# Performance work log

Hardware: AMD Instinct MI355X
Metric: run time of the kernel (lower is better)

Reference implementation:

```python
import jax, jax.numpy as jnp
import numpy as np

B, S, D_IN, D_OUT, H = 4, 2048, 1024, 1024, 16
HD = D_OUT // H  # head_dim = 64


def setup_inputs() -> dict:
    key = jax.random.key(0)
    ks = jax.random.split(key, 6)
    scale = 1.0 / np.sqrt(D_IN)
    return {
        "x": jax.random.normal(ks[0], (B, S, D_IN), dtype=jnp.float32),
        "Wq": jax.random.normal(ks[1], (D_IN, D_OUT), dtype=jnp.float32) * scale,
        "Wk": jax.random.normal(ks[2], (D_IN, D_OUT), dtype=jnp.float32) * scale,
        "Wv": jax.random.normal(ks[3], (D_IN, D_OUT), dtype=jnp.float32) * scale,
        "Wo": jax.random.normal(ks[4], (D_OUT, D_OUT), dtype=jnp.float32) * (1.0 / np.sqrt(D_OUT)),
        "bo": jax.random.normal(ks[5], (D_OUT,), dtype=jnp.float32) * 0.02,
    }


def reference(x, Wq, Wk, Wv, Wo, bo):
    b, n, _ = x.shape
    h, hd = H, HD
    # projections -> (b, h, n, hd)
    q = (x @ Wq).reshape(b, n, h, hd).transpose(0, 2, 1, 3)
    k = (x @ Wk).reshape(b, n, h, hd).transpose(0, 2, 1, 3)
    v = (x @ Wv).reshape(b, n, h, hd).transpose(0, 2, 1, 3)
    # scores (b, h, n, n) with causal mask then scale (matches original order)
    scores = jnp.einsum("bhqd,bhkd->bhqk", q, k)
    causal = jnp.tril(jnp.ones((n, n), dtype=bool))  # True = keep
    scores = jnp.where(causal, scores, -jnp.inf) / jnp.sqrt(jnp.asarray(hd, x.dtype))
    attn = jax.nn.softmax(scores, axis=-1)
    ctx = jnp.einsum("bhqk,bhkd->bhqd", attn, v)
    ctx = ctx.transpose(0, 2, 1, 3).reshape(b, n, h * hd)
    return ctx @ Wo + bo
```

## Files before the change

### kernel.cpp

```cpp
#include <hip/hip_runtime.h>
#include <hip/hip_bf16.h>
#include <math.h>

typedef __attribute__((ext_vector_type(4))) float f32x4;
typedef __attribute__((ext_vector_type(16))) float f32x16;
typedef __attribute__((ext_vector_type(8))) short bf16x8;
typedef __attribute__((ext_vector_type(4))) unsigned int u32x4;

#define DEV __device__ __forceinline__
#define MFMA16 __builtin_amdgcn_mfma_f32_16x16x32_bf16
#define MFMA32 __builtin_amdgcn_mfma_f32_32x32x16_bf16
#define SBAR __builtin_amdgcn_s_barrier()
#define SCHED0 __builtin_amdgcn_sched_barrier(0)

constexpr int S      = 2048;
constexpr int DMODEL = 1024;
constexpr int HD     = 64;
constexpr int MROWS  = 4 * 2048;

DEV unsigned short f2bf(float f) {
  union { float f; unsigned int u; } v; v.f = f;
  unsigned int u = v.u;
  unsigned int r = u + 0x7fffu + ((u >> 16) & 1u);
  return (unsigned short)(r >> 16);
}

DEV unsigned int pkbf(float lo, float hi) {
  __hip_bfloat162 h = __float22bfloat162_rn(float2{lo, hi});
  union { __hip_bfloat162 h; unsigned int u; } c; c.h = h;
  return c.u;
}

DEV void gload_lds16(const void* g, void* l) {
  __builtin_amdgcn_global_load_lds(
      (const __attribute__((address_space(1))) unsigned int*)g,
      (__attribute__((address_space(3))) unsigned int*)l, 16, 0, 0);
}

__global__ __launch_bounds__(256) void k_conv(const float* __restrict__ in,
                                              unsigned short* __restrict__ out) {
  int i = blockIdx.x * 256 + threadIdx.x;
  float4 v = ((const float4*)in)[i];
  ushort4 o;
  o.x = f2bf(v.x); o.y = f2bf(v.y); o.z = f2bf(v.z); o.w = f2bf(v.w);
  ((ushort4*)out)[i] = o;
}

__global__ __launch_bounds__(256) void k_transpose(const float* __restrict__ W,
                                                   unsigned short* __restrict__ Wt) {
  __shared__ float tile[32][33];
  int n0 = blockIdx.x * 32, k0 = blockIdx.y * 32;
  int tx = threadIdx.x, ty = threadIdx.y;
#pragma unroll
  for (int j = 0; j < 4; ++j)
    tile[ty + j * 8][tx] = W[(size_t)(k0 + ty + j * 8) * DMODEL + n0 + tx];
  __syncthreads();
#pragma unroll
  for (int j = 0; j < 4; ++j)
    Wt[(size_t)(n0 + ty + j * 8) * DMODEL + k0 + tx] = f2bf(tile[tx][ty + j * 8]);
}

template<int NBX, int EPI>
__global__ __launch_bounds__(512, 2) void k_gemm8(const unsigned short* __restrict__ A,
                                                  const unsigned short* __restrict__ Bt,
                                                  unsigned short* __restrict__ Qg,
                                                  unsigned short* __restrict__ Kg,
                                                  unsigned short* __restrict__ Vg,
                                                  const float* __restrict__ bo,
                                                  float* __restrict__ out) {
  __shared__ __align__(16) char lds[98304];
  const int tid = threadIdx.x, lane = tid & 63;
  const int wid = tid >> 6, wm = wid >> 1, wn = wid & 1;
  const int lq = lane & 15, lg = lane >> 4;
  const int flat = blockIdx.x;
  const int wg = (flat & 7) * (NBX * 4) + (flat >> 3);
  const int by = wg / NBX, bx = wg % NBX;
  const int m0 = by * 256, n0 = bx * 128;

  auto stage = [&](int kt, int buf) {
    char* dA = lds + buf * 49152;
    char* dB = dA + 32768;
    const unsigned short* gA = A + (size_t)m0 * DMODEL + kt * 64;
    const unsigned short* gB = Bt + (size_t)n0 * DMODEL + kt * 64;
#pragma unroll
    for (int i = 0; i < 4; ++i) {
      int c = tid + i * 512; int r = c >> 3, cc = c & 7;
      gload_lds16(gA + (size_t)r * DMODEL + ((cc ^ (r & 7)) << 3), dA + c * 16);
    }
#pragma unroll
    for (int i = 0; i < 2; ++i) {
      int c = tid + i * 512; int r = c >> 3, cc = c & 7;
      gload_lds16(gB + (size_t)r * DMODEL + ((cc ^ (r & 7)) << 3), dB + c * 16);
    }
  };

  stage(0, 0);
  stage(1, 1);
  SCHED0;
  asm volatile("s_waitcnt vmcnt(6)" ::: "memory");
  SCHED0;
  SBAR;
  SCHED0;

  f32x4 acc[4][4] = {};
#pragma unroll 1
  for (int t = 0; t < 16; ++t) {
    const int cur = t & 1;
    const char* pA = lds + cur * 49152;
    const char* pB = pA + 32768;
    bf16x8 af[4][2], bf[4][2];
#pragma unroll
    for (int kk = 0; kk < 2; ++kk) {
#pragma unroll
      for (int mi = 0; mi < 4; ++mi) {
        int row = wm * 64 + mi * 16 + lq;
        af[mi][kk] = *(const bf16x8*)(pA + row * 128 + ((((kk << 2) + lg) ^ (row & 7)) << 4));
      }
#pragma unroll
      for (int ni = 0; ni < 4; ++ni) {
        int row = wn * 64 + ni * 16 + lq;
        bf[ni][kk] = *(const bf16x8*)(pB + row * 128 + ((((kk << 2) + lg) ^ (row & 7)) << 4));
      }
    }
    asm volatile("s_waitcnt lgkmcnt(0)" ::: "memory");
    SCHED0;
    SBAR;
    SCHED0;
    if (t < 14) stage(t + 2, cur);
    __builtin_amdgcn_s_setprio(1);
#pragma unroll
    for (int kk = 0; kk < 2; ++kk)
#pragma unroll
      for (int mi = 0; mi < 4; ++mi)
#pragma unroll
        for (int ni = 0; ni < 4; ++ni)
          acc[mi][ni] = MFMA16(af[mi][kk], bf[ni][kk], acc[mi][ni], 0, 0, 0);
    __builtin_amdgcn_s_setprio(0);
    SCHED0;
    if (t < 14) {
      asm volatile("s_waitcnt vmcnt(6)" ::: "memory");
    } else if (t == 14) {
      asm volatile("s_waitcnt vmcnt(0)" ::: "memory");
    }
    SCHED0;
    SBAR;
    SCHED0;
  }

  if (EPI == 0) {
#pragma unroll
    for (int mi = 0; mi < 4; ++mi)
#pragma unroll
      for (int ni = 0; ni < 4; ++ni) {
        int n = n0 + wn * 64 + ni * 16 + lq;
        int widx = n >> 10, nn = n & 1023;
        int h = nn >> 6, d = nn & 63;
        unsigned short* dst = (widx == 0) ? Qg : ((widx == 1) ? Kg : Vg);
        float scale = (widx == 0) ? 0.125f : 1.0f;
#pragma unroll
        for (int r = 0; r < 4; ++r) {
          int m = m0 + wm * 64 + mi * 16 + lg * 4 + r;
          int b_ = m >> 11, s_ = m & 2047;
          dst[(size_t)((b_ * 16 + h) * 2048 + s_) * HD + d] = f2bf(acc[mi][ni][r] * scale);
        }
      }
  } else {
#pragma unroll
    for (int mi = 0; mi < 4; ++mi)
#pragma unroll
      for (int ni = 0; ni < 4; ++ni) {
        int n = n0 + wn * 64 + ni * 16 + lq;
        float bv = bo[n];
#pragma unroll
        for (int r = 0; r < 4; ++r) {
          int m = m0 + wm * 64 + mi * 16 + lg * 4 + r;
          out[(size_t)m * DMODEL + n] = acc[mi][ni][r] + bv;
        }
      }
  }
}

__global__ __launch_bounds__(512, 2) void k_attn(const unsigned short* __restrict__ Qg,
                                                 const unsigned short* __restrict__ Kg,
                                                 const unsigned short* __restrict__ Vg,
                                                 unsigned short* __restrict__ Ctx) {
  __shared__ __align__(16) char lds[32768];
  const int pr = blockIdx.x;
  const int bh = blockIdx.y;
  const int tid = threadIdx.x;
  const int lane = tid & 63, w = tid >> 6;
  const int lq5 = lane & 31, hi = lane >> 5;
  const size_t base = (size_t)bh * (S * HD);
  const int b = bh >> 4, h = bh & 15;
  const int vkrow = tid >> 3, vcc = tid & 7;

#pragma unroll 1
  for (int half = 0; half < 2; ++half) {
    const int Qb = half ? (7 - pr) : pr;
    const int q0w = Qb * 256 + w * 32;
    const int tmax = 4 * Qb + 3;
    const int diag = q0w >> 6;

    bf16x8 qF[4];
#pragma unroll
    for (int dc = 0; dc < 4; ++dc)
      qF[dc] = *(const bf16x8*)(Qg + base + (size_t)(q0w + lq5) * HD + dc * 16 + hi * 8);

    f32x16 o0 = {}, o1 = {};
    float m_run = -INFINITY, l_run = 0.f;

    __syncthreads();
    {
      int row = tid >> 3, cc = tid & 7, scc = cc ^ (row & 7);
      gload_lds16(Kg + base + (size_t)row * HD + scc * 8, lds + tid * 16);
      bf16x8 vv = *(const bf16x8*)(Vg + base + (size_t)vkrow * HD + vcc * 8);
#pragma unroll
      for (int j = 0; j < 8; ++j) {
        int d = vcc * 8 + j;
        int fd = (d & 7) ^ ((d >> 3) & 7);
        *(unsigned short*)(lds + 16384 + d * 128 + (((vkrow >> 3) ^ fd) << 4) + (vkrow & 7) * 2) =
            (unsigned short)vv[j];
      }
    }
    __syncthreads();

#pragma unroll 1
    for (int t = 0; t <= tmax; ++t) {
      const int cur = t & 1, nxt = cur ^ 1;
      char* sK  = lds + cur * 8192;
      char* sVT = lds + 16384 + cur * 8192;
      const bool have_next = (t < tmax);
      bf16x8 vv;
      if (have_next) {
        vv = *(const bf16x8*)(Vg + base + (size_t)((t + 1) * 64 + vkrow) * HD + vcc * 8);
        int row = tid >> 3, cc = tid & 7, scc = cc ^ (row & 7);
        gload_lds16(Kg + base + (size_t)((t + 1) * 64 + row) * HD + scc * 8,
                    lds + nxt * 8192 + tid * 16);
      }
      const bool active = (t <= diag);
      if (active) {
        const bool isdiag = (t == diag);
        const int nkb = (isdiag && !(q0w & 32)) ? 1 : 2;
        f32x16 st0 = {}, st1 = {};
#pragma unroll
        for (int dc = 0; dc < 4; ++dc) {
          int row = lq5;
          bf16x8 a0 = *(const bf16x8*)(sK + row * 128 + (((2 * dc + hi) ^ (row & 7)) << 4));
          st0 = MFMA32(a0, qF[dc], st0, 0, 0, 0);
        }
        if (nkb == 2) {
#pragma unroll
          for (int dc = 0; dc < 4; ++dc) {
            int row = 32 + lq5;
            bf16x8 a1 = *(const bf16x8*)(sK + row * 128 + (((2 * dc + hi) ^ (row & 7)) << 4));
            st1 = MFMA32(a1, qF[dc], st1, 0, 0, 0);
          }
        }
        if (isdiag) {
          int qo = q0w + lq5 - t * 64;
          if (q0w & 32) {
#pragma unroll
            for (int r = 0; r < 16; ++r) {
              int key = 32 + (r & 3) + 8 * (r >> 2) + 4 * hi;
              st1[r] = (key > qo) ? -INFINITY : st1[r];
            }
          } else {
#pragma unroll
            for (int r = 0; r < 16; ++r) {
              int key = (r & 3) + 8 * (r >> 2) + 4 * hi;
              st0[r] = (key > qo) ? -INFINITY : st0[r];
            }
          }
        }
        float mx = st0[0];
#pragma unroll
        for (int r = 1; r < 16; ++r) mx = fmaxf(mx, st0[r]);
        if (nkb == 2) {
#pragma unroll
          for (int r = 0; r < 16; ++r) mx = fmaxf(mx, st1[r]);
        }
        mx = fmaxf(mx, __shfl_xor(mx, 32));
        bool need = !(mx <= m_run + 8.0f);
        if (__any(need)) {
          float mn = fmaxf(m_run, mx);
          float alpha = __expf(m_run - mn);
          m_run = mn;
          l_run *= alpha;
#pragma unroll
          for (int r = 0; r < 16; ++r) { o0[r] *= alpha; o1[r] *= alpha; }
        }
        float rs[4] = {0.f, 0.f, 0.f, 0.f};
#pragma unroll
        for (int r = 0; r < 16; ++r) {
          float p = __expf(st0[r] - m_run);
          st0[r] = p;
          rs[r & 3] += p;
        }
        if (nkb == 2) {
#pragma unroll
          for (int r = 0; r < 16; ++r) {
            float p = __expf(st1[r] - m_run);
            st1[r] = p;
            rs[r & 3] += p;
          }
        }
        float rsum = (rs[0] + rs[1]) + (rs[2] + rs[3]);
        rsum += __shfl_xor(rsum, 32);
        l_run += rsum;
        {
          unsigned int wv[8];
#pragma unroll
          for (int j = 0; j < 8; ++j) wv[j] = pkbf(st0[2 * j], st0[2 * j + 1]);
          asm("v_permlane32_swap_b32 %0, %1" : "+v"(wv[0]), "+v"(wv[2]));
          asm("v_permlane32_swap_b32 %0, %1" : "+v"(wv[1]), "+v"(wv[3]));
          asm("v_permlane32_swap_b32 %0, %1" : "+v"(wv[4]), "+v"(wv[6]));
          asm("v_permlane32_swap_b32 %0, %1" : "+v"(wv[5]), "+v"(wv[7]));
          union { bf16x8 v; unsigned int u[4]; } fa, fb;
          fa.u[0] = wv[0]; fa.u[1] = wv[1]; fa.u[2] = wv[2]; fa.u[3] = wv[3];
          fb.u[0] = wv[4]; fb.u[1] = wv[5]; fb.u[2] = wv[6]; fb.u[3] = wv[7];
#pragma unroll
          for (int kc = 0; kc < 2; ++kc) {
            bf16x8 bp = kc ? fb.v : fa.v;
            {
              int d = lq5, fd = (d & 7) ^ ((d >> 3) & 7);
              bf16x8 av = *(const bf16x8*)(sVT + d * 128 + (((kc * 2 + hi) ^ fd) << 4));
              o0 = MFMA32(av, bp, o0, 0, 0, 0);
            }
            {
              int d = 32 + lq5, fd = (d & 7) ^ ((d >> 3) & 7);
              bf16x8 av = *(const bf16x8*)(sVT + d * 128 + (((kc * 2 + hi) ^ fd) << 4));
              o1 = MFMA32(av, bp, o1, 0, 0, 0);
            }
          }
        }
        if (nkb == 2) {
          unsigned int wv[8];
#pragma unroll
          for (int j = 0; j < 8; ++j) wv[j] = pkbf(st1[2 * j], st1[2 * j + 1]);
          asm("v_permlane32_swap_b32 %0, %1" : "+v"(wv[0]), "+v"(wv[2]));
          asm("v_permlane32_swap_b32 %0, %1" : "+v"(wv[1]), "+v"(wv[3]));
          asm("v_permlane32_swap_b32 %0, %1" : "+v"(wv[4]), "+v"(wv[6]));
          asm("v_permlane32_swap_b32 %0, %1" : "+v"(wv[5]), "+v"(wv[7]));
          union { bf16x8 v; unsigned int u[4]; } fa, fb;
          fa.u[0] = wv[0]; fa.u[1] = wv[1]; fa.u[2] = wv[2]; fa.u[3] = wv[3];
          fb.u[0] = wv[4]; fb.u[1] = wv[5]; fb.u[2] = wv[6]; fb.u[3] = wv[7];
#pragma unroll
          for (int kc = 0; kc < 2; ++kc) {
            bf16x8 bp = kc ? fb.v : fa.v;
            {
              int d = lq5, fd = (d & 7) ^ ((d >> 3) & 7);
              bf16x8 av = *(const bf16x8*)(sVT + d * 128 + ((((2 + kc) * 2 + hi) ^ fd) << 4));
              o0 = MFMA32(av, bp, o0, 0, 0, 0);
            }
            {
              int d = 32 + lq5, fd = (d & 7) ^ ((d >> 3) & 7);
              bf16x8 av = *(const bf16x8*)(sVT + d * 128 + ((((2 + kc) * 2 + hi) ^ fd) << 4));
              o1 = MFMA32(av, bp, o1, 0, 0, 0);
            }
          }
        }
      }
      if (have_next) {
        char* dVT = lds + 16384 + nxt * 8192;
#pragma unroll
        for (int j = 0; j < 8; ++j) {
          int d = vcc * 8 + j;
          int fd = (d & 7) ^ ((d >> 3) & 7);
          *(unsigned short*)(dVT + d * 128 + (((vkrow >> 3) ^ fd) << 4) + (vkrow & 7) * 2) =
              (unsigned short)vv[j];
        }
      }
      __syncthreads();
    }

    __syncthreads();
    {
      float inv = 1.0f / l_run;
      char* slice = lds + w * 4096;
#pragma unroll
      for (int db = 0; db < 2; ++db)
#pragma unroll
        for (int j = 0; j < 8; ++j) {
          int d0 = (j & 1) * 2 + (j >> 1) * 8 + 4 * hi + 32 * db;
          float va = (db ? o1[2 * j] : o0[2 * j]) * inv;
          float vb = (db ? o1[2 * j + 1] : o0[2 * j + 1]) * inv;
          *(unsigned int*)(slice + lq5 * 128 + (((d0 >> 3) ^ (lq5 & 7)) << 4) + (d0 & 7) * 2) =
              pkbf(va, vb);
        }
      asm volatile("s_waitcnt lgkmcnt(0)" ::: "memory");
#pragma unroll
      for (int i = 0; i < 4; ++i) {
        int r = lane >> 1, cc = (lane & 1) * 4 + i;
        u32x4 v = *(const u32x4*)(slice + r * 128 + ((cc ^ (r & 7)) << 4));
        *(u32x4*)(Ctx + (size_t)(b * S + q0w + r) * DMODEL + h * HD + cc * 8) = v;
      }
    }
  }
}

extern "C" void kernel_launch(void* const* d_in, const int* in_sizes, int n_in,
                              void* d_out, int out_size, void* d_ws, size_t ws_size,
                              hipStream_t stream) {
  const float* x  = (const float*)d_in[0];
  const float* Wq = (const float*)d_in[1];
  const float* Wk = (const float*)d_in[2];
  const float* Wv = (const float*)d_in[3];
  const float* Wo = (const float*)d_in[4];
  const float* bo = (const float*)d_in[5];
  float* out = (float*)d_out;

  char* p = (char*)d_ws;
  unsigned short* xb  = (unsigned short*)p; p += (size_t)MROWS * DMODEL * 2;
  unsigned short* wt  = (unsigned short*)p; p += (size_t)3 * DMODEL * DMODEL * 2;
  unsigned short* wot = (unsigned short*)p; p += (size_t)DMODEL * DMODEL * 2;
  unsigned short* qg  = (unsigned short*)p; p += (size_t)MROWS * DMODEL * 2;
  unsigned short* kg  = (unsigned short*)p; p += (size_t)MROWS * DMODEL * 2;
  unsigned short* vg  = (unsigned short*)p; p += (size_t)MROWS * DMODEL * 2;
  unsigned short* ctx = (unsigned short*)p; p += (size_t)MROWS * DMODEL * 2;

  k_conv<<<(MROWS * DMODEL) / 1024, 256, 0, stream>>>(x, xb);
  dim3 tb(32, 8), tg(32, 32);
  k_transpose<<<tg, tb, 0, stream>>>(Wq, wt);
  k_transpose<<<tg, tb, 0, stream>>>(Wk, wt + (size_t)DMODEL * DMODEL);
  k_transpose<<<tg, tb, 0, stream>>>(Wv, wt + (size_t)2 * DMODEL * DMODEL);
  k_transpose<<<tg, tb, 0, stream>>>(Wo, wot);
  k_gemm8<24, 0><<<768, 512, 0, stream>>>(xb, wt, qg, kg, vg, nullptr, nullptr);
  k_attn<<<dim3(4, 64), 512, 0, stream>>>(qg, kg, vg, ctx);
  k_gemm8<8, 1><<<256, 512, 0, stream>>>(ctx, wot, nullptr, nullptr, nullptr, bo, out);
}
```

Baseline: 192.1 us.

## Split attention blocks into half-size CTAs, use exp2 softmax, raise MFMA priority

The attention kernel moves from 512-thread blocks over 256 query rows to 256-thread blocks over 128 query rows, launching twice as many blocks. Each thread now loads two K/V chunks per tile. The aim is finer load balance across the causal triangle and higher occupancy, at the cost of each block reloading K/V tiles that used to be shared by twice as many queries. The Q scale now folds in log2(e) so softmax can use exp2f, and s_setprio brackets the MFMA sections to favour matrix issue across waves.

```diff
diff --git a/kernel.cpp b/kernel.cpp
--- a/kernel.cpp
+++ b/kernel.cpp
@@ -156,7 +156,7 @@
         int widx = n >> 10, nn = n & 1023;
         int h = nn >> 6, d = nn & 63;
         unsigned short* dst = (widx == 0) ? Qg : ((widx == 1) ? Kg : Vg);
-        float scale = (widx == 0) ? 0.125f : 1.0f;
+        float scale = (widx == 0) ? 0.18033688f : 1.0f;
 #pragma unroll
         for (int r = 0; r < 4; ++r) {
           int m = m0 + wm * 64 + mi * 16 + lg * 4 + r;
@@ -180,24 +180,24 @@
   }
 }
 
-__global__ __launch_bounds__(512, 2) void k_attn(const unsigned short* __restrict__ Qg,
+__global__ __launch_bounds__(256, 4) void k_attn(const unsigned short* __restrict__ Qg,
                                                  const unsigned short* __restrict__ Kg,
                                                  const unsigned short* __restrict__ Vg,
                                                  unsigned short* __restrict__ Ctx) {
   __shared__ __align__(16) char lds[32768];
-  const int pr = blockIdx.x;
+  const int pr = blockIdx.x >> 1;
+  const int sub = blockIdx.x & 1;
   const int bh = blockIdx.y;
   const int tid = threadIdx.x;
   const int lane = tid & 63, w = tid >> 6;
   const int lq5 = lane & 31, hi = lane >> 5;
   const size_t base = (size_t)bh * (S * HD);
   const int b = bh >> 4, h = bh & 15;
-  const int vkrow = tid >> 3, vcc = tid & 7;
 
 #pragma unroll 1
   for (int half = 0; half < 2; ++half) {
     const int Qb = half ? (7 - pr) : pr;
-    const int q0w = Qb * 256 + w * 32;
+    const int q0w = Qb * 256 + sub * 128 + w * 32;
     const int tmax = 4 * Qb + 3;
     const int diag = q0w >> 6;
 
@@ -210,15 +210,22 @@
     float m_run = -INFINITY, l_run = 0.f;
 
     __syncthreads();
-    {
-      int row = tid >> 3, cc = tid & 7, scc = cc ^ (row & 7);
-      gload_lds16(Kg + base + (size_t)row * HD + scc * 8, lds + tid * 16);
-      bf16x8 vv = *(const bf16x8*)(Vg + base + (size_t)vkrow * HD + vcc * 8);
+#pragma unroll
+    for (int i = 0; i < 2; ++i) {
+      int c = tid + i * 256;
+      int row = c >> 3, cc = c & 7, scc = cc ^ (row & 7);
+      gload_lds16(Kg + base + (size_t)row * HD + scc * 8, lds + c * 16);
+    }
+#pragma unroll
+    for (int i = 0; i < 2; ++i) {
+      int c = tid + i * 256;
+      int krow = c >> 3, vcc = c & 7;
+      bf16x8 vv = *(const bf16x8*)(Vg + base + (size_t)krow * HD + vcc * 8);
 #pragma unroll
       for (int j = 0; j < 8; ++j) {
         int d = vcc * 8 + j;
         int fd = (d & 7) ^ ((d >> 3) & 7);
-        *(unsigned short*)(lds + 16384 + d * 128 + (((vkrow >> 3) ^ fd) << 4) + (vkrow & 7) * 2) =
+        *(unsigned short*)(lds + 16384 + d * 128 + (((krow >> 3) ^ fd) << 4) + (krow & 7) * 2) =
             (unsigned short)vv[j];
       }
     }
@@ -230,18 +237,28 @@
       char* sK  = lds + cur * 8192;
       char* sVT = lds + 16384 + cur * 8192;
       const bool have_next = (t < tmax);
-      bf16x8 vv;
+      bf16x8 vv[2];
       if (have_next) {
-        vv = *(const bf16x8*)(Vg + base + (size_t)((t + 1) * 64 + vkrow) * HD + vcc * 8);
-        int row = tid >> 3, cc = tid & 7, scc = cc ^ (row & 7);
-        gload_lds16(Kg + base + (size_t)((t + 1) * 64 + row) * HD + scc * 8,
-                    lds + nxt * 8192 + tid * 16);
+#pragma unroll
+        for (int i = 0; i < 2; ++i) {
+          int c = tid + i * 256;
+          int krow = c >> 3, vcc = c & 7;
+          vv[i] = *(const bf16x8*)(Vg + base + (size_t)((t + 1) * 64 + krow) * HD + vcc * 8);
+        }
+#pragma unroll
+        for (int i = 0; i < 2; ++i) {
+          int c = tid + i * 256;
+          int row = c >> 3, cc = c & 7, scc = cc ^ (row & 7);
+          gload_lds16(Kg + base + (size_t)((t + 1) * 64 + row) * HD + scc * 8,
+                      lds + nxt * 8192 + c * 16);
+        }
       }
       const bool active = (t <= diag);
       if (active) {
         const bool isdiag = (t == diag);
         const int nkb = (isdiag && !(q0w & 32)) ? 1 : 2;
         f32x16 st0 = {}, st1 = {};
+        __builtin_amdgcn_s_setprio(1);
 #pragma unroll
         for (int dc = 0; dc < 4; ++dc) {
           int row = lq5;
@@ -256,6 +273,7 @@
             st1 = MFMA32(a1, qF[dc], st1, 0, 0, 0);
           }
         }
+        __builtin_amdgcn_s_setprio(0);
         if (isdiag) {
           int qo = q0w + lq5 - t * 64;
           if (q0w & 32) {
@@ -283,7 +301,7 @@
         bool need = !(mx <= m_run + 8.0f);
         if (__any(need)) {
           float mn = fmaxf(m_run, mx);
-          float alpha = __expf(m_run - mn);
+          float alpha = exp2f(m_run - mn);
           m_run = mn;
           l_run *= alpha;
 #pragma unroll
@@ -292,14 +310,14 @@
         float rs[4] = {0.f, 0.f, 0.f, 0.f};
 #pragma unroll
         for (int r = 0; r < 16; ++r) {
-          float p = __expf(st0[r] - m_run);
+          float p = exp2f(st0[r] - m_run);
           st0[r] = p;
           rs[r & 3] += p;
         }
         if (nkb == 2) {
 #pragma unroll
           for (int r = 0; r < 16; ++r) {
-            float p = __expf(st1[r] - m_run);
+            float p = exp2f(st1[r] - m_run);
             st1[r] = p;
             rs[r & 3] += p;
           }
@@ -318,6 +336,7 @@
           union { bf16x8 v; unsigned int u[4]; } fa, fb;
           fa.u[0] = wv[0]; fa.u[1] = wv[1]; fa.u[2] = wv[2]; fa.u[3] = wv[3];
           fb.u[0] = wv[4]; fb.u[1] = wv[5]; fb.u[2] = wv[6]; fb.u[3] = wv[7];
+          __builtin_amdgcn_s_setprio(1);
 #pragma unroll
           for (int kc = 0; kc < 2; ++kc) {
             bf16x8 bp = kc ? fb.v : fa.v;
@@ -332,6 +351,7 @@
               o1 = MFMA32(av, bp, o1, 0, 0, 0);
             }
           }
+          __builtin_amdgcn_s_setprio(0);
         }
         if (nkb == 2) {
           unsigned int wv[8];
@@ -344,6 +364,7 @@
           union { bf16x8 v; unsigned int u[4]; } fa, fb;
           fa.u[0] = wv[0]; fa.u[1] = wv[1]; fa.u[2] = wv[2]; fa.u[3] = wv[3];
           fb.u[0] = wv[4]; fb.u[1] = wv[5]; fb.u[2] = wv[6]; fb.u[3] = wv[7];
+          __builtin_amdgcn_s_setprio(1);
 #pragma unroll
           for (int kc = 0; kc < 2; ++kc) {
             bf16x8 bp = kc ? fb.v : fa.v;
@@ -358,16 +379,22 @@
               o1 = MFMA32(av, bp, o1, 0, 0, 0);
             }
           }
+          __builtin_amdgcn_s_setprio(0);
         }
       }
       if (have_next) {
         char* dVT = lds + 16384 + nxt * 8192;
 #pragma unroll
-        for (int j = 0; j < 8; ++j) {
-          int d = vcc * 8 + j;
-          int fd = (d & 7) ^ ((d >> 3) & 7);
-          *(unsigned short*)(dVT + d * 128 + (((vkrow >> 3) ^ fd) << 4) + (vkrow & 7) * 2) =
-              (unsigned short)vv[j];
+        for (int i = 0; i < 2; ++i) {
+          int c = tid + i * 256;
+          int krow = c >> 3, vcc = c & 7;
+#pragma unroll
+          for (int j = 0; j < 8; ++j) {
+            int d = vcc * 8 + j;
+            int fd = (d & 7) ^ ((d >> 3) & 7);
+            *(unsigned short*)(dVT + d * 128 + (((krow >> 3) ^ fd) << 4) + (krow & 7) * 2) =
+                (unsigned short)vv[i][j];
+          }
         }
       }
       __syncthreads();
@@ -425,6 +452,6 @@
   k_transpose<<<tg, tb, 0, stream>>>(Wv, wt + (size_t)2 * DMODEL * DMODEL);
   k_transpose<<<tg, tb, 0, stream>>>(Wo, wot);
   k_gemm8<24, 0><<<768, 512, 0, stream>>>(xb, wt, qg, kg, vg, nullptr, nullptr);
-  k_attn<<<dim3(4, 64), 512, 0, stream>>>(qg, kg, vg, ctx);
+  k_attn<<<dim3(8, 64), 256, 0, stream>>>(qg, kg, vg, ctx);
   k_gemm8<8, 1><<<256, 512, 0, stream>>>(ctx, wot, nullptr, nullptr, nullptr, bo, out);
 }
```

Measured after the change: 317.1 us. 1.65x slower.

## Use 1024-thread attention blocks with split K/V loaders, exp2 softmax and MFMA priority

Applied to the files above, without the earlier changes.

Attention blocks now hold 16 waves covering a 512-row query block, replacing the previous scheme where each block processed two paired 256-row halves in sequence. The K tile is loaded by the first half of the threads and the V tile is transposed into LDS by the second half. The Q scale now folds in log2(e), so the softmax uses exp2f instead of __expf, and s_setprio brackets raise wave priority around the MFMA sections. This removes the causal load-balancing pairing, so blocks with larger query indices carry more work, and blocks are now twice as large.

```diff
diff --git a/kernel.cpp b/kernel.cpp
--- a/kernel.cpp
+++ b/kernel.cpp
@@ -156,7 +156,7 @@
         int widx = n >> 10, nn = n & 1023;
         int h = nn >> 6, d = nn & 63;
         unsigned short* dst = (widx == 0) ? Qg : ((widx == 1) ? Kg : Vg);
-        float scale = (widx == 0) ? 0.125f : 1.0f;
+        float scale = (widx == 0) ? 0.18033688f : 1.0f;
 #pragma unroll
         for (int r = 0; r < 4; ++r) {
           int m = m0 + wm * 64 + mi * 16 + lg * 4 + r;
@@ -180,220 +180,226 @@
   }
 }
 
-__global__ __launch_bounds__(512, 2) void k_attn(const unsigned short* __restrict__ Qg,
-                                                 const unsigned short* __restrict__ Kg,
-                                                 const unsigned short* __restrict__ Vg,
-                                                 unsigned short* __restrict__ Ctx) {
-  __shared__ __align__(16) char lds[32768];
-  const int pr = blockIdx.x;
+__global__ __launch_bounds__(1024, 4) void k_attn(const unsigned short* __restrict__ Qg,
+                                                  const unsigned short* __restrict__ Kg,
+                                                  const unsigned short* __restrict__ Vg,
+                                                  unsigned short* __restrict__ Ctx) {
+  __shared__ __align__(16) char lds[65536];
+  const int Qb = blockIdx.x;
   const int bh = blockIdx.y;
   const int tid = threadIdx.x;
   const int lane = tid & 63, w = tid >> 6;
   const int lq5 = lane & 31, hi = lane >> 5;
   const size_t base = (size_t)bh * (S * HD);
   const int b = bh >> 4, h = bh & 15;
-  const int vkrow = tid >> 3, vcc = tid & 7;
+
+  const bool isV = (tid >= 512);
+  const int c = tid & 511;
+  const int krow = c >> 3, cc = c & 7;
+  const int scc = cc ^ (krow & 7);
+
+  const int q0w = Qb * 512 + w * 32;
+  const int tmax = 8 * Qb + 7;
+  const int diag = q0w >> 6;
+
+  bf16x8 qF[4];
+#pragma unroll
+  for (int dc = 0; dc < 4; ++dc)
+    qF[dc] = *(const bf16x8*)(Qg + base + (size_t)(q0w + lq5) * HD + dc * 16 + hi * 8);
+
+  f32x16 o0 = {}, o1 = {};
+  float m_run = -INFINITY, l_run = 0.f;
+
+  if (!isV) {
+    gload_lds16(Kg + base + (size_t)krow * HD + scc * 8, lds + c * 16);
+  } else {
+    bf16x8 vv = *(const bf16x8*)(Vg + base + (size_t)krow * HD + cc * 8);
+#pragma unroll
+    for (int j = 0; j < 8; ++j) {
+      int d = cc * 8 + j;
+      int fd = (d & 7) ^ ((d >> 3) & 7);
+      *(unsigned short*)(lds + 16384 + d * 128 + (((krow >> 3) ^ fd) << 4) + (krow & 7) * 2) =
+          (unsigned short)vv[j];
+    }
+  }
+  __syncthreads();
 
 #pragma unroll 1
-  for (int half = 0; half < 2; ++half) {
-    const int Qb = half ? (7 - pr) : pr;
-    const int q0w = Qb * 256 + w * 32;
-    const int tmax = 4 * Qb + 3;
-    const int diag = q0w >> 6;
-
-    bf16x8 qF[4];
-#pragma unroll
-    for (int dc = 0; dc < 4; ++dc)
-      qF[dc] = *(const bf16x8*)(Qg + base + (size_t)(q0w + lq5) * HD + dc * 16 + hi * 8);
-
-    f32x16 o0 = {}, o1 = {};
-    float m_run = -INFINITY, l_run = 0.f;
-
+  for (int t = 0; t <= tmax; ++t) {
+    const int cur = t & 1, nxt = cur ^ 1;
+    char* sK  = lds + cur * 8192;
+    char* sVT = lds + 16384 + cur * 8192;
+    const bool have_next = (t < tmax);
+    bf16x8 vv;
+    if (have_next) {
+      if (!isV)
+        gload_lds16(Kg + base + (size_t)((t + 1) * 64 + krow) * HD + scc * 8,
+                    lds + nxt * 8192 + c * 16);
+      else
+        vv = *(const bf16x8*)(Vg + base + (size_t)((t + 1) * 64 + krow) * HD + cc * 8);
+    }
+    const bool active = (t <= diag);
+    if (active) {
+      const bool isdiag = (t == diag);
+      const int nkb = (isdiag && !(q0w & 32)) ? 1 : 2;
+      f32x16 st0 = {}, st1 = {};
+      __builtin_amdgcn_s_setprio(1);
+#pragma unroll
+      for (int dc = 0; dc < 4; ++dc) {
+        int row = lq5;
+        bf16x8 a0 = *(const bf16x8*)(sK + row * 128 + (((2 * dc + hi) ^ (row & 7)) << 4));
+        st0 = MFMA32(a0, qF[dc], st0, 0, 0, 0);
+      }
+      if (nkb == 2) {
+#pragma unroll
+        for (int dc = 0; dc < 4; ++dc) {
+          int row = 32 + lq5;
+          bf16x8 a1 = *(const bf16x8*)(sK + row * 128 + (((2 * dc + hi) ^ (row & 7)) << 4));
+          st1 = MFMA32(a1, qF[dc], st1, 0, 0, 0);
+        }
+      }
+      __builtin_amdgcn_s_setprio(0);
+      if (isdiag) {
+        int qo = q0w + lq5 - t * 64;
+        if (q0w & 32) {
+#pragma unroll
+          for (int r = 0; r < 16; ++r) {
+            int key = 32 + (r & 3) + 8 * (r >> 2) + 4 * hi;
+            st1[r] = (key > qo) ? -INFINITY : st1[r];
+          }
+        } else {
+#pragma unroll
+          for (int r = 0; r < 16; ++r) {
+            int key = (r & 3) + 8 * (r >> 2) + 4 * hi;
+            st0[r] = (key > qo) ? -INFINITY : st0[r];
+          }
+        }
+      }
+      float mx = st0[0];
+#pragma unroll
+      for (int r = 1; r < 16; ++r) mx = fmaxf(mx, st0[r]);
+      if (nkb == 2) {
+#pragma unroll
+        for (int r = 0; r < 16; ++r) mx = fmaxf(mx, st1[r]);
+      }
+      mx = fmaxf(mx, __shfl_xor(mx, 32));
+      bool need = !(mx <= m_run + 8.0f);
+      if (__any(need)) {
+        float mn = fmaxf(m_run, mx);
+        float alpha = exp2f(m_run - mn);
+        m_run = mn;
+        l_run *= alpha;
+#pragma unroll
+        for (int r = 0; r < 16; ++r) { o0[r] *= alpha; o1[r] *= alpha; }
+      }
+      float rs[4] = {0.f, 0.f, 0.f, 0.f};
+#pragma unroll
+      for (int r = 0; r < 16; ++r) {
+        float p = exp2f(st0[r] - m_run);
+        st0[r] = p;
+        rs[r & 3] += p;
+      }
+      if (nkb == 2) {
+#pragma unroll
+        for (int r = 0; r < 16; ++r) {
+          float p = exp2f(st1[r] - m_run);
+          st1[r] = p;
+          rs[r & 3] += p;
+        }
+      }
+      float rsum = (rs[0] + rs[1]) + (rs[2] + rs[3]);
+      rsum += __shfl_xor(rsum, 32);
+      l_run += rsum;
+      {
+        unsigned int wv[8];
+#pragma unroll
+        for (int j = 0; j < 8; ++j) wv[j] = pkbf(st0[2 * j], st0[2 * j + 1]);
+        asm("v_permlane32_swap_b32 %0, %1" : "+v"(wv[0]), "+v"(wv[2]));
+        asm("v_permlane32_swap_b32 %0, %1" : "+v"(wv[1]), "+v"(wv[3]));
+        asm("v_permlane32_swap_b32 %0, %1" : "+v"(wv[4]), "+v"(wv[6]));
+        asm("v_permlane32_swap_b32 %0, %1" : "+v"(wv[5]), "+v"(wv[7]));
+        union { bf16x8 v; unsigned int u[4]; } fa, fb;
+        fa.u[0] = wv[0]; fa.u[1] = wv[1]; fa.u[2] = wv[2]; fa.u[3] = wv[3];
+        fb.u[0] = wv[4]; fb.u[1] = wv[5]; fb.u[2] = wv[6]; fb.u[3] = wv[7];
+        __builtin_amdgcn_s_setprio(1);
+#pragma unroll
+        for (int kc = 0; kc < 2; ++kc) {
+          bf16x8 bp = kc ? fb.v : fa.v;
+          {
+            int d = lq5, fd = (d & 7) ^ ((d >> 3) & 7);
+            bf16x8 av = *(const bf16x8*)(sVT + d * 128 + (((kc * 2 + hi) ^ fd) << 4));
+            o0 = MFMA32(av, bp, o0, 0, 0, 0);
+          }
+          {
+            int d = 32 + lq5, fd = (d & 7) ^ ((d >> 3) & 7);
+            bf16x8 av = *(const bf16x8*)(sVT + d * 128 + (((kc * 2 + hi) ^ fd) << 4));
+            o1 = MFMA32(av, bp, o1, 0, 0, 0);
+          }
+        }
+        __builtin_amdgcn_s_setprio(0);
+      }
+      if (nkb == 2) {
+        unsigned int wv[8];
+#pragma unroll
+        for (int j = 0; j < 8; ++j) wv[j] = pkbf(st1[2 * j], st1[2 * j + 1]);
+        asm("v_permlane32_swap_b32 %0, %1" : "+v"(wv[0]), "+v"(wv[2]));
+        asm("v_permlane32_swap_b32 %0, %1" : "+v"(wv[1]), "+v"(wv[3]));
+        asm("v_permlane32_swap_b32 %0, %1" : "+v"(wv[4]), "+v"(wv[6]));
+        asm("v_permlane32_swap_b32 %0, %1" : "+v"(wv[5]), "+v"(wv[7]));
+        union { bf16x8 v; unsigned int u[4]; } fa, fb;
+        fa.u[0] = wv[0]; fa.u[1] = wv[1]; fa.u[2] = wv[2]; fa.u[3] = wv[3];
+        fb.u[0] = wv[4]; fb.u[1] = wv[5]; fb.u[2] = wv[6]; fb.u[3] = wv[7];
+        __builtin_amdgcn_s_setprio(1);
+#pragma unroll
+        for (int kc = 0; kc < 2; ++kc) {
+          bf16x8 bp = kc ? fb.v : fa.v;
+          {
+            int d = lq5, fd = (d & 7) ^ ((d >> 3) & 7);
+            bf16x8 av = *(const bf16x8*)(sVT + d * 128 + ((((2 + kc) * 2 + hi) ^ fd) << 4));
+            o0 = MFMA32(av, bp, o0, 0, 0, 0);
+          }
+          {
+            int d = 32 + lq5, fd = (d & 7) ^ ((d >> 3) & 7);
+            bf16x8 av = *(const bf16x8*)(sVT + d * 128 + ((((2 + kc) * 2 + hi) ^ fd) << 4));
+            o1 = MFMA32(av, bp, o1, 0, 0, 0);
+          }
+        }
+        __builtin_amdgcn_s_setprio(0);
+      }
+    }
+    if (have_next && isV) {
+      char* dVT = lds + 16384 + nxt * 8192;
+#pragma unroll
+      for (int j = 0; j < 8; ++j) {
+        int d = cc * 8 + j;
+        int fd = (d & 7) ^ ((d >> 3) & 7);
+        *(unsigned short*)(dVT + d * 128 + (((krow >> 3) ^ fd) << 4) + (krow & 7) * 2) =
+            (unsigned short)vv[j];
+      }
+    }
     __syncthreads();
-    {
-      int row = tid >> 3, cc = tid & 7, scc = cc ^ (row & 7);
-      gload_lds16(Kg + base + (size_t)row * HD + scc * 8, lds + tid * 16);
-      bf16x8 vv = *(const bf16x8*)(Vg + base + (size_t)vkrow * HD + vcc * 8);
+  }
+
+  __syncthreads();
+  {
+    float inv = 1.0f / l_run;
+    char* slice = lds + w * 4096;
+#pragma unroll
+    for (int db = 0; db < 2; ++db)
 #pragma unroll
       for (int j = 0; j < 8; ++j) {
-        int d = vcc * 8 + j;
-        int fd = (d & 7) ^ ((d >> 3) & 7);
-        *(unsigned short*)(lds + 16384 + d * 128 + (((vkrow >> 3) ^ fd) << 4) + (vkrow & 7) * 2) =
-            (unsigned short)vv[j];
-      }
-    }
-    __syncthreads();
-
-#pragma unroll 1
-    for (int t = 0; t <= tmax; ++t) {
-      const int cur = t & 1, nxt = cur ^ 1;
-      char* sK  = lds + cur * 8192;
-      char* sVT = lds + 16384 + cur * 8192;
-      const bool have_next = (t < tmax);
-      bf16x8 vv;
-      if (have_next) {
-        vv = *(const bf16x8*)(Vg + base + (size_t)((t + 1) * 64 + vkrow) * HD + vcc * 8);
-        int row = tid >> 3, cc = tid & 7, scc = cc ^ (row & 7);
-        gload_lds16(Kg + base + (size_t)((t + 1) * 64 + row) * HD + scc * 8,
-                    lds + nxt * 8192 + tid * 16);
-      }
-      const bool active = (t <= diag);
-      if (active) {
-        const bool isdiag = (t == diag);
-        const int nkb = (isdiag && !(q0w & 32)) ? 1 : 2;
-        f32x16 st0 = {}, st1 = {};
-#pragma unroll
-        for (int dc = 0; dc < 4; ++dc) {
-          int row = lq5;
-          bf16x8 a0 = *(const bf16x8*)(sK + row * 128 + (((2 * dc + hi) ^ (row & 7)) << 4));
-          st0 = MFMA32(a0, qF[dc], st0, 0, 0, 0);
-        }
-        if (nkb == 2) {
-#pragma unroll
-          for (int dc = 0; dc < 4; ++dc) {
-            int row = 32 + lq5;
-            bf16x8 a1 = *(const bf16x8*)(sK + row * 128 + (((2 * dc + hi) ^ (row & 7)) << 4));
-            st1 = MFMA32(a1, qF[dc], st1, 0, 0, 0);
-          }
-        }
-        if (isdiag) {
-          int qo = q0w + lq5 - t * 64;
-          if (q0w & 32) {
-#pragma unroll
-            for (int r = 0; r < 16; ++r) {
-              int key = 32 + (r & 3) + 8 * (r >> 2) + 4 * hi;
-              st1[r] = (key > qo) ? -INFINITY : st1[r];
-            }
-          } else {
-#pragma unroll
-            for (int r = 0; r < 16; ++r) {
-              int key = (r & 3) + 8 * (r >> 2) + 4 * hi;
-              st0[r] = (key > qo) ? -INFINITY : st0[r];
-            }
-          }
-        }
-        float mx = st0[0];
-#pragma unroll
-        for (int r = 1; r < 16; ++r) mx = fmaxf(mx, st0[r]);
-        if (nkb == 2) {
-#pragma unroll
-          for (int r = 0; r < 16; ++r) mx = fmaxf(mx, st1[r]);
-        }
-        mx = fmaxf(mx, __shfl_xor(mx, 32));
-        bool need = !(mx <= m_run + 8.0f);
-        if (__any(need)) {
-          float mn = fmaxf(m_run, mx);
-          float alpha = __expf(m_run - mn);
-          m_run = mn;
-          l_run *= alpha;
-#pragma unroll
-          for (int r = 0; r < 16; ++r) { o0[r] *= alpha; o1[r] *= alpha; }
-        }
-        float rs[4] = {0.f, 0.f, 0.f, 0.f};
-#pragma unroll
-        for (int r = 0; r < 16; ++r) {
-          float p = __expf(st0[r] - m_run);
-          st0[r] = p;
-          rs[r & 3] += p;
-        }
-        if (nkb == 2) {
-#pragma unroll
-          for (int r = 0; r < 16; ++r) {
-            float p = __expf(st1[r] - m_run);
-            st1[r] = p;
-            rs[r & 3] += p;
-          }
-        }
-        float rsum = (rs[0] + rs[1]) + (rs[2] + rs[3]);
-        rsum += __shfl_xor(rsum, 32);
-        l_run += rsum;
-        {
-          unsigned int wv[8];
-#pragma unroll
-          for (int j = 0; j < 8; ++j) wv[j] = pkbf(st0[2 * j], st0[2 * j + 1]);
-          asm("v_permlane32_swap_b32 %0, %1" : "+v"(wv[0]), "+v"(wv[2]));
-          asm("v_permlane32_swap_b32 %0, %1" : "+v"(wv[1]), "+v"(wv[3]));
-          asm("v_permlane32_swap_b32 %0, %1" : "+v"(wv[4]), "+v"(wv[6]));
-          asm("v_permlane32_swap_b32 %0, %1" : "+v"(wv[5]), "+v"(wv[7]));
-          union { bf16x8 v; unsigned int u[4]; } fa, fb;
-          fa.u[0] = wv[0]; fa.u[1] = wv[1]; fa.u[2] = wv[2]; fa.u[3] = wv[3];
-          fb.u[0] = wv[4]; fb.u[1] = wv[5]; fb.u[2] = wv[6]; fb.u[3] = wv[7];
-#pragma unroll
-          for (int kc = 0; kc < 2; ++kc) {
-            bf16x8 bp = kc ? fb.v : fa.v;
-            {
-              int d = lq5, fd = (d & 7) ^ ((d >> 3) & 7);
-              bf16x8 av = *(const bf16x8*)(sVT + d * 128 + (((kc * 2 + hi) ^ fd) << 4));
-              o0 = MFMA32(av, bp, o0, 0, 0, 0);
-            }
-            {
-              int d = 32 + lq5, fd = (d & 7) ^ ((d >> 3) & 7);
-              bf16x8 av = *(const bf16x8*)(sVT + d * 128 + (((kc * 2 + hi) ^ fd) << 4));
-              o1 = MFMA32(av, bp, o1, 0, 0, 0);
-            }
-          }
-        }
-        if (nkb == 2) {
-          unsigned int wv[8];
-#pragma unroll
-          for (int j = 0; j < 8; ++j) wv[j] = pkbf(st1[2 * j], st1[2 * j + 1]);
-          asm("v_permlane32_swap_b32 %0, %1" : "+v"(wv[0]), "+v"(wv[2]));
-          asm("v_permlane32_swap_b32 %0, %1" : "+v"(wv[1]), "+v"(wv[3]));
-          asm("v_permlane32_swap_b32 %0, %1" : "+v"(wv[4]), "+v"(wv[6]));
-          asm("v_permlane32_swap_b32 %0, %1" : "+v"(wv[5]), "+v"(wv[7]));
-          union { bf16x8 v; unsigned int u[4]; } fa, fb;
-          fa.u[0] = wv[0]; fa.u[1] = wv[1]; fa.u[2] = wv[2]; fa.u[3] = wv[3];
-          fb.u[0] = wv[4]; fb.u[1] = wv[5]; fb.u[2] = wv[6]; fb.u[3] = wv[7];
-#pragma unroll
-          for (int kc = 0; kc < 2; ++kc) {
-            bf16x8 bp = kc ? fb.v : fa.v;
-            {
-              int d = lq5, fd = (d & 7) ^ ((d >> 3) & 7);
-              bf16x8 av = *(const bf16x8*)(sVT + d * 128 + ((((2 + kc) * 2 + hi) ^ fd) << 4));
-              o0 = MFMA32(av, bp, o0, 0, 0, 0);
-            }
-            {
-              int d = 32 + lq5, fd = (d & 7) ^ ((d >> 3) & 7);
-              bf16x8 av = *(const bf16x8*)(sVT + d * 128 + ((((2 + kc) * 2 + hi) ^ fd) << 4));
-              o1 = MFMA32(av, bp, o1, 0, 0, 0);
-            }
-          }
-        }
-      }
-      if (have_next) {
-        char* dVT = lds + 16384 + nxt * 8192;
-#pragma unroll
-        for (int j = 0; j < 8; ++j) {
-          int d = vcc * 8 + j;
-          int fd = (d & 7) ^ ((d >> 3) & 7);
-          *(unsigned short*)(dVT + d * 128 + (((vkrow >> 3) ^ fd) << 4) + (vkrow & 7) * 2) =
-              (unsigned short)vv[j];
-        }
-      }
-      __syncthreads();
-    }
-
-    __syncthreads();
-    {
-      float inv = 1.0f / l_run;
-      char* slice = lds + w * 4096;
-#pragma unroll
-      for (int db = 0; db < 2; ++db)
-#pragma unroll
-        for (int j = 0; j < 8; ++j) {
-          int d0 = (j & 1) * 2 + (j >> 1) * 8 + 4 * hi + 32 * db;
-          float va = (db ? o1[2 * j] : o0[2 * j]) * inv;
-          float vb = (db ? o1[2 * j + 1] : o0[2 * j + 1]) * inv;
-          *(unsigned int*)(slice + lq5 * 128 + (((d0 >> 3) ^ (lq5 & 7)) << 4) + (d0 & 7) * 2) =
-              pkbf(va, vb);
-        }
-      asm volatile("s_waitcnt lgkmcnt(0)" ::: "memory");
-#pragma unroll
-      for (int i = 0; i < 4; ++i) {
-        int r = lane >> 1, cc = (lane & 1) * 4 + i;
-        u32x4 v = *(const u32x4*)(slice + r * 128 + ((cc ^ (r & 7)) << 4));
-        *(u32x4*)(Ctx + (size_t)(b * S + q0w + r) * DMODEL + h * HD + cc * 8) = v;
-      }
+        int d0 = (j & 1) * 2 + (j >> 1) * 8 + 4 * hi + 32 * db;
+        float va = (db ? o1[2 * j] : o0[2 * j]) * inv;
+        float vb = (db ? o1[2 * j + 1] : o0[2 * j + 1]) * inv;
+        *(unsigned int*)(slice + lq5 * 128 + (((d0 >> 3) ^ (lq5 & 7)) << 4) + (d0 & 7) * 2) =
+            pkbf(va, vb);
+      }
+    asm volatile("s_waitcnt lgkmcnt(0)" ::: "memory");
+#pragma unroll
+    for (int i = 0; i < 4; ++i) {
+      int r = lane >> 1, cc2 = (lane & 1) * 4 + i;
+      u32x4 v = *(const u32x4*)(slice + r * 128 + ((cc2 ^ (r & 7)) << 4));
+      *(u32x4*)(Ctx + (size_t)(b * S + q0w + r) * DMODEL + h * HD + cc2 * 8) = v;
     }
   }
 }
@@ -425,6 +431,6 @@
   k_transpose<<<tg, tb, 0, stream>>>(Wv, wt + (size_t)2 * DMODEL * DMODEL);
   k_transpose<<<tg, tb, 0, stream>>>(Wo, wot);
   k_gemm8<24, 0><<<768, 512, 0, stream>>>(xb, wt, qg, kg, vg, nullptr, nullptr);
-  k_attn<<<dim3(4, 64), 512, 0, stream>>>(qg, kg, vg, ctx);
+  k_attn<<<dim3(4, 64), 1024, 0, stream>>>(qg, kg, vg, ctx);
   k_gemm8<8, 1><<<256, 512, 0, stream>>>(ctx, wot, nullptr, nullptr, nullptr, bo, out);
 }
```

After: 237.7 us. 23.7% more time.
